# Kernel optimization log

Measured on AMD Instinct MI355X. Metric: run time of the kernel, lower is better.

The kernel has to match this reference:

```python
import jax, jax.numpy as jnp
import numpy as np

P = 8.0  # Lp norm order for NormDist layers (finite-p distance conv)
CHUNK = 8  # output-channel chunk for memory-bounded distance computation
EPS = 8.0 / 255.0


def lp_norm(d, p=P):
    # stable Lp norm over last axis: m * (sum((d/m)^p))^(1/p)
    m = jnp.max(d, axis=-1)
    ms = jnp.where(m > 0, m, 1.0)
    s = jnp.sum((d / ms[..., None]) ** p, axis=-1)
    ss = jnp.where(m > 0, s, 1.0)
    return m * ss ** (1.0 / p)


def extract_patches(t, k, s, pad):
    # [B,C,H,W] -> [B, L, C*k*k] (torch-unfold channel-major ordering), L=Ho*Wo
    pt = jax.lax.conv_general_dilated_patches(t, (k, k), (s, s), [(pad, pad), (pad, pad)])
    B, F, Ho, Wo = pt.shape
    return pt.reshape(B, F, Ho * Wo).transpose(0, 2, 1), Ho, Wo


def normdist_conv(c, lo, hi, w, k, s, pad):
    # Lp-distance conv with interval bound propagation on (center, lower, upper)
    pc, Ho, Wo = extract_patches(c, k, s, pad)
    pl, _, _ = extract_patches(lo, k, s, pad)
    ph, _, _ = extract_patches(hi, k, s, pad)
    O = w.shape[0]
    wf = w.reshape(O, -1)  # [O, F]

    def per_chunk(wc):  # wc: [CHUNK, F]
        dc = jnp.abs(pc[:, :, None, :] - wc)                     # [B,L,CHUNK,F]
        oc = lp_norm(dc)
        # per-element distance bounds given lo <= x <= hi
        dl = jnp.maximum(jnp.maximum(pl[:, :, None, :] - wc, wc - ph[:, :, None, :]), 0.0)
        ol = lp_norm(dl)
        dh = jnp.maximum(jnp.abs(pl[:, :, None, :] - wc), jnp.abs(ph[:, :, None, :] - wc))
        oh = lp_norm(dh)
        return oc, ol, oh

    oc, ol, oh = jax.lax.map(per_chunk, wf.reshape(O // CHUNK, CHUNK, -1))

    def to_img(t):  # [nch, B, L, CHUNK] -> [B, O, Ho, Wo]
        nch, B, L, ch = t.shape
        return t.transpose(1, 0, 3, 2).reshape(B, nch * ch, Ho, Wo)

    return to_img(oc), to_img(ol), to_img(oh)


def bound_relu(c, lo, hi):
    return jax.nn.relu(c), jax.nn.relu(lo), jax.nn.relu(hi)


def _mp(t):
    return jax.lax.reduce_window(t, -jnp.inf, jax.lax.max, (1, 1, 3, 3), (1, 1, 2, 2), 'VALID')


def bound_maxpool(c, lo, hi):
    return _mp(c), _mp(lo), _mp(hi)


def bound_linear(c, lo, hi, W, b=None):
    oc = c @ W.T
    mid = ((lo + hi) * 0.5) @ W.T
    rad = ((hi - lo) * 0.5) @ jnp.abs(W).T
    if b is not None:
        oc = oc + b
        mid = mid + b
    return oc, mid - rad, mid + rad


def setup_inputs() -> dict:
    key = jax.random.key(0)
    ks = jax.random.split(key, 10)
    x = jax.random.normal(ks[0], (16, 3, 32, 32), jnp.float32)
    lower = x - EPS
    upper = x + EPS
    w1 = jax.random.normal(ks[1], (96, 3, 7, 7), jnp.float32)
    w2 = jax.random.normal(ks[2], (256, 96, 5, 5), jnp.float32)
    w3 = jax.random.normal(ks[3], (384, 256, 3, 3), jnp.float32)
    w4 = jax.random.normal(ks[4], (384, 384, 3, 3), jnp.float32)
    w5 = jax.random.normal(ks[5], (256, 384, 3, 3), jnp.float32)
    fw1 = jax.random.normal(ks[6], (1024, 2304), jnp.float32) * 0.02
    fw2 = jax.random.normal(ks[7], (512, 1024), jnp.float32) * 0.03
    fw3 = jax.random.normal(ks[8], (10, 512), jnp.float32) * 0.04
    fb3 = jax.random.normal(ks[9], (10,), jnp.float32)
    return {"x": x, "lower": lower, "upper": upper, "w1": w1, "w2": w2, "w3": w3,
            "w4": w4, "w5": w5, "fw1": fw1, "fw2": fw2, "fw3": fw3, "fb3": fb3}


def reference(x, lower, upper, w1, w2, w3, w4, w5, fw1, fw2, fw3, fb3):
    c, l, u = normdist_conv(x, lower, upper, w1, 7, 2, 2)   # 32 -> 15
    c, l, u = bound_relu(c, l, u)
    c, l, u = bound_maxpool(c, l, u)                        # 15 -> 7
    c, l, u = normdist_conv(c, l, u, w2, 5, 1, 2)           # 7 -> 7
    c, l, u = bound_relu(c, l, u)
    c, l, u = bound_maxpool(c, l, u)                        # 7 -> 3
    c, l, u = normdist_conv(c, l, u, w3, 3, 1, 1)
    c, l, u = bound_relu(c, l, u)
    c, l, u = normdist_conv(c, l, u, w4, 3, 1, 1)
    c, l, u = bound_relu(c, l, u)
    c, l, u = normdist_conv(c, l, u, w5, 3, 1, 1)
    c, l, u = bound_relu(c, l, u)
    B = c.shape[0]
    c, l, u = c.reshape(B, -1), l.reshape(B, -1), u.reshape(B, -1)
    c, l, u = bound_linear(c, l, u, fw1)
    c, l, u = bound_relu(c, l, u)
    c, l, u = bound_linear(c, l, u, fw2)
    c, l, u = bound_relu(c, l, u)
    c, l, u = bound_linear(c, l, u, fw3, fb3)
    # final negation swaps the roles of lower/upper
    return (-c, -u, -l)
```

## Files before the change

### kernel.cpp

```cpp
#include <hip/hip_runtime.h>
#include <math.h>


__device__ __forceinline__ float rt8(float s) { return sqrtf(sqrtf(sqrtf(s))); }

__device__ __forceinline__ void tap16(float w, float pc, float pl, float pu,
                                      float& aC, float& aL, float& aH)
{
    float a = pc - w; float a2 = a * a, a4 = a2 * a2; aC = fmaf(a4, a4, aC);
    float x = pl - w, y = pu - w;
    float dl = fmaxf(fmaxf(x, -y), 0.f);
    float e2 = dl * dl, e4 = e2 * e2; aL = fmaf(e4, e4, aL);
    float h2 = fmaxf(x * x, y * y);
    float h4 = h2 * h2; aH = fmaf(h4, h4, aH);
}

__launch_bounds__(256)
__global__ void wtrans4(const float* __restrict__ W2, const float* __restrict__ W3,
                        const float* __restrict__ W4, const float* __restrict__ W5,
                        float* __restrict__ T2, float* __restrict__ T3,
                        float* __restrict__ T4, float* __restrict__ T5)
{
    constexpr int nt2 = 4 * 38, nt3 = 6 * 36, nt4 = 6 * 54, nt5 = 4 * 54;
    int bid = blockIdx.x;
    const float* W; float* T; int O, CK, t;
    if (bid < nt2)                   { W = W2; T = T2; O = 256; CK = 2400; t = bid; }
    else if (bid < nt2 + nt3)        { W = W3; T = T3; O = 384; CK = 2304; t = bid - nt2; }
    else if (bid < nt2 + nt3 + nt4)  { W = W4; T = T4; O = 384; CK = 3456; t = bid - nt2 - nt3; }
    else                             { W = W5; T = T5; O = 256; CK = 3456; t = bid - nt2 - nt3 - nt4; }
    int tilesC = (CK + 63) / 64;
    int to = t / tilesC, tc = t - to * tilesC;
    int o0 = to * 64, c0 = tc * 64;
    __shared__ float tile[64][65];
    int lane = threadIdx.x & 63, wv = threadIdx.x >> 6;
    #pragma unroll
    for (int i = 0; i < 16; ++i) {
        int row = wv + i * 4;
        int c = c0 + lane;
        tile[row][lane] = (c < CK) ? W[(size_t)(o0 + row) * CK + c] : 0.f;
    }
    __syncthreads();
    #pragma unroll
    for (int i = 0; i < 16; ++i) {
        int row = wv + i * 4;
        int c = c0 + row;
        if (c < CK) T[(size_t)c * O + o0 + lane] = tile[lane][row];
    }
}

template<int K, int S, int PAD, int CC, int HIN, int WIN, int HO, int WO>
__launch_bounds__(256)
__global__ void conv_a(const float* __restrict__ IC, const float* __restrict__ IL,
                       const float* __restrict__ IU, const float* __restrict__ W,
                       float* __restrict__ OUT, int B, int Cin, int O, int OG)
{
    constexpr int PH = (HO - 1) * S + K;
    constexpr int PW = (WO - 1) * S + K;
    constexpr int PP = PH * PW;
    constexpr int HW = HIN * WIN;
    constexpr int NP = HO * WO;
    constexpr int ROUNDS = (NP + 63) / 64;
    __shared__ float lds[CC * 3 * PP];

    int og = blockIdx.x % OG;
    int b  = (blockIdx.x / OG) % B;
    int tid = threadIdx.x;

    for (int i = tid; i < CC * 3 * PP; i += 256) lds[i] = 0.f;
    __syncthreads();
    for (int tsel = 0; tsel < 3; ++tsel) {
        const float* src = (tsel == 0 ? IC : (tsel == 1 ? IL : IU))
                         + (size_t)b * Cin * HW;
        for (int e = tid; e < CC * HW; e += 256) {
            int c = e / HW, p = e % HW;
            int pr = p / WIN, pw_ = p % WIN;
            lds[c * 3 * PP + tsel * PP + (pr + PAD) * PW + (pw_ + PAD)] = src[e];
        }
    }
    __syncthreads();

    int wave = tid >> 6, lane = tid & 63;
    int o = __builtin_amdgcn_readfirstlane(og * 4 + wave);
    const float* wp = W + (size_t)o * Cin * (K * K);

    for (int r = 0; r < ROUNDS; ++r) {
        int pos = r * 64 + lane;
        bool act = pos < NP;
        int pp = act ? pos : 0;
        int oh = pp / WO, ow = pp % WO;
        const float* sl = lds + (oh * S) * PW + ow * S;
        const float* wc = wp;
        float aC = 0.f, aL = 0.f, aH = 0.f;
        for (int c = 0; c < CC; ++c) {
            #pragma unroll
            for (int kh = 0; kh < K; ++kh)
                #pragma unroll
                for (int kw = 0; kw < K; ++kw) {
                    float w = wc[kh * K + kw];
                    tap16(w, sl[kh * PW + kw], sl[PP + kh * PW + kw],
                          sl[2 * PP + kh * PW + kw], aC, aL, aH);
                }
            sl += 3 * PP; wc += K * K;
        }
        if (act) {
            size_t N = (size_t)B * O * NP;
            size_t oidx = ((size_t)b * O + o) * NP + pos;
            OUT[oidx] = aC; OUT[N + oidx] = aL; OUT[2 * N + oidx] = aH;
        }
    }
}

__global__ void pool_rt8(const float* __restrict__ in, float* __restrict__ out,
                         int BC, int Hin, int Win, int Ho, int Wo,
                         int n_in, int n_out)
{
    int idx = blockIdx.x * blockDim.x + threadIdx.x;
    int per = BC * Ho * Wo;
    if (idx >= 3 * per) return;
    int tsel = idx / per; int r = idx - tsel * per;
    int ow = r % Wo; int t2 = r / Wo;
    int oh = t2 % Ho; int bc = t2 / Ho;
    const float* ip = in + (size_t)tsel * n_in + (size_t)bc * Hin * Win;
    int ih0 = oh * 2, iw0 = ow * 2;
    float m = -INFINITY;
    #pragma unroll
    for (int i = 0; i < 3; ++i)
        #pragma unroll
        for (int j = 0; j < 3; ++j)
            m = fmaxf(m, ip[(ih0 + i) * Win + (iw0 + j)]);
    out[(size_t)tsel * n_out + r] = rt8(m);
}

template<int CC>
__launch_bounds__(256)
__global__ void conv2_kernel(const float* __restrict__ IN, const float* __restrict__ WT,
                             float* __restrict__ P, int nin)
{
    constexpr int B = 16, Cin = 96, O = 256;
    constexpr size_t N = (size_t)B * O * 49;
    __shared__ __align__(16) float slab[CC * 180];
    int x = blockIdx.x;
    int oh   = x % 7;
    int b    = (x / 7) % B;
    int chunk = x / (7 * B);
    int c0 = chunk * CC;
    int tid = threadIdx.x;

    for (int i = tid; i < CC * 180; i += 256) {
        int c = i / 180; int rem = i - c * 180;
        int tsel = rem / 60; int rr = rem - tsel * 60;
        int r = rr / 12, col = rr - r * 12;
        int ih = oh + r - 2, iw = col - 2;
        float v = 0.f;
        if (col < 11 && (unsigned)ih < 7u && (unsigned)iw < 7u)
            v = IN[(size_t)tsel * nin + ((size_t)b * Cin + c0 + c) * 49 + ih * 7 + iw];
        slab[i] = v;
    }
    __syncthreads();

    int o = tid;
    float aC[7], aL[7], aH[7];
    #pragma unroll
    for (int u = 0; u < 7; ++u) { aC[u] = 0.f; aL[u] = 0.f; aH[u] = 0.f; }

    for (int c = 0; c < CC; ++c) {
        const float* wp = WT + (size_t)((c0 + c) * 25) * O + o;
        float w[25];
        #pragma unroll
        for (int t = 0; t < 25; ++t) w[t] = wp[(size_t)t * O];
        const float* sb = slab + c * 180;
        #pragma unroll
        for (int r = 0; r < 5; ++r) {
            float X[12], L[12], U[12];
            const float4* px = (const float4*)(sb + r * 12);
            const float4* pl = (const float4*)(sb + 60 + r * 12);
            const float4* pu = (const float4*)(sb + 120 + r * 12);
            ((float4*)X)[0] = px[0]; ((float4*)X)[1] = px[1]; ((float4*)X)[2] = px[2];
            ((float4*)L)[0] = pl[0]; ((float4*)L)[1] = pl[1]; ((float4*)L)[2] = pl[2];
            ((float4*)U)[0] = pu[0]; ((float4*)U)[1] = pu[1]; ((float4*)U)[2] = pu[2];
            #pragma unroll
            for (int ow = 0; ow < 7; ++ow)
                #pragma unroll
                for (int kw = 0; kw < 5; ++kw)
                    tap16(w[r * 5 + kw], X[ow + kw], L[ow + kw], U[ow + kw],
                          aC[ow], aL[ow], aH[ow]);
        }
    }

    float* Pc = P + (size_t)chunk * 3 * N;
    size_t rowbase = ((size_t)(b * 7 + oh) * 7) * O + o;
    #pragma unroll
    for (int u = 0; u < 7; ++u) {
        Pc[rowbase + (size_t)u * O]         = aC[u];
        Pc[N + rowbase + (size_t)u * O]     = aL[u];
        Pc[2 * N + rowbase + (size_t)u * O] = aH[u];
    }
}

__global__ void comb2_pool2(const float* __restrict__ P, float* __restrict__ D)
{
    constexpr int B = 16, O = 256, NCH = 16;
    constexpr size_t N = (size_t)B * O * 49;
    int idx = blockIdx.x * blockDim.x + threadIdx.x;
    if (idx >= 3 * B * 9 * O) return;
    int o = idx & 255; int t = idx >> 8;
    int pos = t % 9; t /= 9;
    int b = t % B; int tsel = t / B;
    int ph = pos / 3, pw = pos % 3;
    float m = 0.f;
    #pragma unroll
    for (int i = 0; i < 3; ++i)
        #pragma unroll
        for (int j = 0; j < 3; ++j) {
            int sp = (ph * 2 + i) * 7 + (pw * 2 + j);
            size_t base = (size_t)tsel * N + ((size_t)b * 49 + sp) * O + o;
            float s = 0.f;
            #pragma unroll
            for (int ch = 0; ch < NCH; ++ch) s += P[(size_t)ch * 3 * N + base];
            m = fmaxf(m, s);
        }
    D[idx] = rt8(m);
}

template<int CC>
__launch_bounds__(384)
__global__ void conv3x3_kernel(const float* __restrict__ IN, const float* __restrict__ WT,
                               float* __restrict__ P, int B, int Cin, int O)
{
    __shared__ float slab[CC * 75];
    int x = blockIdx.x;
    int b = x % B;
    int chunk = x / B;
    int c0 = chunk * CC;
    int tid = threadIdx.x;

    for (int i = tid; i < CC * 75; i += blockDim.x) {
        int c = i / 75; int rem = i - c * 75;
        int tsel = rem / 25; int rr = rem - tsel * 25;
        int iy = rr / 5, ix = rr - iy * 5;
        int ih = iy - 1, iw = ix - 1;
        float v = 0.f;
        if ((unsigned)ih < 3u && (unsigned)iw < 3u)
            v = IN[(((size_t)tsel * B + b) * 9 + (ih * 3 + iw)) * Cin + (c0 + c)];
        slab[i] = v;
    }
    __syncthreads();

    int o = tid;
    float aC[9], aL[9], aH[9];
    #pragma unroll
    for (int u = 0; u < 9; ++u) { aC[u] = 0.f; aL[u] = 0.f; aH[u] = 0.f; }

    for (int c = 0; c < CC; ++c) {
        const float* wp = WT + (size_t)((c0 + c) * 9) * O + o;
        float w[9];
        #pragma unroll
        for (int t = 0; t < 9; ++t) w[t] = wp[(size_t)t * O];
        const float* sb = slab + c * 75;
        #pragma unroll
        for (int py = 0; py < 3; ++py)
            #pragma unroll
            for (int px = 0; px < 3; ++px)
                #pragma unroll
                for (int ky = 0; ky < 3; ++ky)
                    #pragma unroll
                    for (int kx = 0; kx < 3; ++kx) {
                        int iy = py + ky, ix = px + kx;
                        tap16(w[ky * 3 + kx], sb[iy * 5 + ix], sb[25 + iy * 5 + ix],
                              sb[50 + iy * 5 + ix],
                              aC[py * 3 + px], aL[py * 3 + px], aH[py * 3 + px]);
                    }
    }

    size_t N = (size_t)B * O * 9;
    float* Pc = P + (size_t)chunk * 3 * N;
    size_t base = ((size_t)b * 9) * O + o;
    #pragma unroll
    for (int u = 0; u < 9; ++u) {
        Pc[base + (size_t)u * O]         = aC[u];
        Pc[N + base + (size_t)u * O]     = aL[u];
        Pc[2 * N + base + (size_t)u * O] = aH[u];
    }
}

__global__ void conv_comb_flat(const float* __restrict__ P, float* __restrict__ OUT,
                               size_t N3, int NCH)
{
    size_t idx = (size_t)blockIdx.x * blockDim.x + threadIdx.x;
    if (idx >= N3) return;
    float s = 0.f;
    for (int ch = 0; ch < NCH; ++ch) s += P[(size_t)ch * N3 + idx];
    OUT[idx] = rt8(s);
}

__global__ void comb5_std(const float* __restrict__ P, float* __restrict__ G, int NCH)
{
    constexpr int B = 16, O = 256;
    constexpr size_t N = (size_t)B * O * 9;
    size_t idx = (size_t)blockIdx.x * blockDim.x + threadIdx.x;
    if (idx >= 3 * N) return;
    float s = 0.f;
    for (int ch = 0; ch < NCH; ++ch) s += P[(size_t)ch * 3 * N + idx];
    int o = (int)(idx % O); size_t t = idx / O;
    int pos = (int)(t % 9); t /= 9;
    int b = (int)(t % B); int tsel = (int)(t / B);
    G[(size_t)tsel * N + ((size_t)b * O + o) * 9 + pos] = rt8(s);
}

__launch_bounds__(256)
__global__ void fc_gemv(const float* __restrict__ IC, const float* __restrict__ IL,
                        const float* __restrict__ IU, const float* __restrict__ W,
                        float* __restrict__ OUT, int B, int In, int Out)
{
    int gw = (int)((blockIdx.x * blockDim.x + threadIdx.x) >> 6);
    int lane = threadIdx.x & 63;
    if (gw >= B * Out) return;
    int o = gw % Out, b = gw / Out;
    const float4* wr = (const float4*)(W  + (size_t)o * In);
    const float4* cr = (const float4*)(IC + (size_t)b * In);
    const float4* lr = (const float4*)(IL + (size_t)b * In);
    const float4* ur = (const float4*)(IU + (size_t)b * In);
    int In4 = In >> 2;
    float sc = 0.f, sm = 0.f, sr = 0.f;
    for (int i = lane; i < In4; i += 64) {
        float4 w4 = wr[i], c4 = cr[i], l4 = lr[i], u4 = ur[i];
        sc = fmaf(c4.x, w4.x, sc); sc = fmaf(c4.y, w4.y, sc);
        sc = fmaf(c4.z, w4.z, sc); sc = fmaf(c4.w, w4.w, sc);
        sm = fmaf((l4.x + u4.x) * 0.5f, w4.x, sm);
        sm = fmaf((l4.y + u4.y) * 0.5f, w4.y, sm);
        sm = fmaf((l4.z + u4.z) * 0.5f, w4.z, sm);
        sm = fmaf((l4.w + u4.w) * 0.5f, w4.w, sm);
        sr = fmaf((u4.x - l4.x) * 0.5f, fabsf(w4.x), sr);
        sr = fmaf((u4.y - l4.y) * 0.5f, fabsf(w4.y), sr);
        sr = fmaf((u4.z - l4.z) * 0.5f, fabsf(w4.z), sr);
        sr = fmaf((u4.w - l4.w) * 0.5f, fabsf(w4.w), sr);
    }
    #pragma unroll
    for (int off = 32; off; off >>= 1) {
        sc += __shfl_xor(sc, off);
        sm += __shfl_xor(sm, off);
        sr += __shfl_xor(sr, off);
    }
    if (lane == 0) {
        size_t N = (size_t)B * Out;
        size_t idx = (size_t)b * Out + o;
        OUT[idx]         = fmaxf(sc, 0.f);
        OUT[N + idx]     = fmaxf(sm - sr, 0.f);
        OUT[2 * N + idx] = fmaxf(sm + sr, 0.f);
    }
}

__global__ void bound_linear_kernel(
    const float* __restrict__ IC, const float* __restrict__ IL, const float* __restrict__ IU,
    const float* __restrict__ W, const float* __restrict__ bias,
    float* __restrict__ OC, float* __restrict__ OL, float* __restrict__ OU,
    int B, int In, int Out)
{
    int idx = blockIdx.x * blockDim.x + threadIdx.x;
    if (idx >= B * Out) return;
    int o = idx % Out, b = idx / Out;
    const float* wr = W  + (size_t)o * In;
    const float* cr = IC + (size_t)b * In;
    const float* lr = IL + (size_t)b * In;
    const float* ur = IU + (size_t)b * In;
    float sc = 0.f, sm = 0.f, sr = 0.f;
    for (int i = 0; i < In; ++i) {
        float w = wr[i];
        sc = fmaf(cr[i], w, sc);
        sm = fmaf((lr[i] + ur[i]) * 0.5f, w, sm);
        sr = fmaf((ur[i] - lr[i]) * 0.5f, fabsf(w), sr);
    }
    float bb = bias[o]; sc += bb; sm += bb;
    OC[idx] = -sc; OL[idx] = -(sm - sr); OU[idx] = -(sm + sr);
}

extern "C" void kernel_launch(void* const* d_in, const int* in_sizes, int n_in,
                              void* d_out, int out_size, void* d_ws, size_t ws_size,
                              hipStream_t stream)
{
    const float* x   = (const float*)d_in[0];
    const float* lo  = (const float*)d_in[1];
    const float* hi  = (const float*)d_in[2];
    const float* w1  = (const float*)d_in[3];
    const float* w2  = (const float*)d_in[4];
    const float* w3  = (const float*)d_in[5];
    const float* w4  = (const float*)d_in[6];
    const float* w5  = (const float*)d_in[7];
    const float* fw1 = (const float*)d_in[8];
    const float* fw2 = (const float*)d_in[9];
    const float* fw3 = (const float*)d_in[10];
    const float* fb3 = (const float*)d_in[11];
    float* out = (float*)d_out;
    float* ws  = (float*)d_ws;

    const size_t n_c1 = 16u * 96 * 15 * 15;
    const size_t n_p1 = 16u * 96 * 7 * 7;
    const size_t n_d  = 16u * 256 * 9;
    const size_t n_c3 = 16u * 384 * 9;
    const size_t n_c5 = 16u * 256 * 9;
    const size_t n_f1 = 16u * 1024;
    const size_t n_f2 = 16u * 512;

    float* A   = ws;
    float* Bp  = A  + 3 * n_c1;
    float* D   = Bp + 3 * n_p1;
    float* E   = D  + 3 * n_d;
    float* F   = E  + 3 * n_c3;
    float* G   = F  + 3 * n_c3;
    float* H   = G  + 3 * n_c5;
    float* I   = H  + 3 * n_f1;
    float* WT2 = I  + 3 * n_f2;
    float* WT3 = WT2 + 614400;
    float* WT4 = WT3 + 884736;
    float* WT5 = WT4 + 1327104;
    float* SP  = WT5 + 884736;

    const int BS = 256;
    auto grid = [](size_t tot) { return dim3((unsigned)((tot + 255) / 256)); };

    wtrans4<<<4 * 38 + 6 * 36 + 6 * 54 + 4 * 54, BS, 0, stream>>>(
        w2, w3, w4, w5, WT2, WT3, WT4, WT5);

    conv_a<7, 2, 2, 3, 32, 32, 15, 15><<<384, BS, 0, stream>>>(
        x, lo, hi, w1, A, 16, 3, 96, 24);
    pool_rt8<<<grid(3 * n_p1), BS, 0, stream>>>(
        A, Bp, 16 * 96, 15, 15, 7, 7, (int)n_c1, (int)n_p1);
    conv2_kernel<6><<<16 * 16 * 7, 256, 0, stream>>>(Bp, WT2, SP, (int)n_p1);
    comb2_pool2<<<grid(3 * n_d), BS, 0, stream>>>(SP, D);
    conv3x3_kernel<8><<<32 * 16, 384, 0, stream>>>(D, WT3, SP, 16, 256, 384);
    conv_comb_flat<<<grid(3 * n_c3), BS, 0, stream>>>(SP, E, 3 * n_c3, 32);
    conv3x3_kernel<8><<<48 * 16, 384, 0, stream>>>(E, WT4, SP, 16, 384, 384);
    conv_comb_flat<<<grid(3 * n_c3), BS, 0, stream>>>(SP, F, 3 * n_c3, 48);
    conv3x3_kernel<8><<<48 * 16, 256, 0, stream>>>(F, WT5, SP, 16, 384, 256);
    comb5_std<<<grid(3 * n_c5), BS, 0, stream>>>(SP, G, 48);
    fc_gemv<<<grid(16384u * 64), BS, 0, stream>>>(
        G, G + n_c5, G + 2 * n_c5, fw1, H, 16, 2304, 1024);
    fc_gemv<<<grid(8192u * 64), BS, 0, stream>>>(
        H, H + n_f1, H + 2 * n_f1, fw2, I, 16, 1024, 512);
    bound_linear_kernel<<<grid(160), BS, 0, stream>>>(
        I, I + n_f2, I + 2 * n_f2, fw3, fb3,
        out, out + 320, out + 160, 16, 512, 10);
}
```

Baseline: 655.0 us.

## Pack channel pairs into float2 lanes to use packed FP32 math in conv kernels

Weights are transposed into a channel-pair interleaved layout and the input slabs are stored with adjacent channels interleaved. The conv2 and 3x3 kernels then process two input channels per iteration with 2-wide vector types, which lets the compiler emit packed FP32 instructions (v_pk_fma/v_pk_mul). The two lanes are summed at the end. This relies on CC being even and changes the weight layout, and it raises register use for the vector accumulators.

```diff
diff --git a/kernel.cpp b/kernel.cpp
--- a/kernel.cpp
+++ b/kernel.cpp
@@ -1,6 +1,8 @@
 #include <hip/hip_runtime.h>
 #include <math.h>
 
+
+typedef float vf2 __attribute__((ext_vector_type(2)));
 
 __device__ __forceinline__ float rt8(float s) { return sqrtf(sqrtf(sqrtf(s))); }
 
@@ -15,6 +17,21 @@
     float h4 = h2 * h2; aH = fmaf(h4, h4, aH);
 }
 
+__device__ __forceinline__ void tap16v2(vf2 w, vf2 pc, vf2 pl, vf2 pu,
+                                        vf2& aC, vf2& aL, vf2& aH)
+{
+    vf2 a = pc - w; vf2 a2 = a * a, a4 = a2 * a2;
+    aC = __builtin_elementwise_fma(a4, a4, aC);
+    vf2 x = pl - w, y = pu - w;
+    vf2 zero = {0.f, 0.f};
+    vf2 dl = __builtin_elementwise_max(__builtin_elementwise_max(x, -y), zero);
+    vf2 e2 = dl * dl, e4 = e2 * e2;
+    aL = __builtin_elementwise_fma(e4, e4, aL);
+    vf2 h2 = __builtin_elementwise_max(x * x, y * y);
+    vf2 h4 = h2 * h2;
+    aH = __builtin_elementwise_fma(h4, h4, aH);
+}
+
 __launch_bounds__(256)
 __global__ void wtrans4(const float* __restrict__ W2, const float* __restrict__ W3,
                         const float* __restrict__ W4, const float* __restrict__ W5,
@@ -23,11 +40,11 @@
 {
     constexpr int nt2 = 4 * 38, nt3 = 6 * 36, nt4 = 6 * 54, nt5 = 4 * 54;
     int bid = blockIdx.x;
-    const float* W; float* T; int O, CK, t;
-    if (bid < nt2)                   { W = W2; T = T2; O = 256; CK = 2400; t = bid; }
-    else if (bid < nt2 + nt3)        { W = W3; T = T3; O = 384; CK = 2304; t = bid - nt2; }
-    else if (bid < nt2 + nt3 + nt4)  { W = W4; T = T4; O = 384; CK = 3456; t = bid - nt2 - nt3; }
-    else                             { W = W5; T = T5; O = 256; CK = 3456; t = bid - nt2 - nt3 - nt4; }
+    const float* W; float* T; int O, CK, KK, t;
+    if (bid < nt2)                   { W = W2; T = T2; O = 256; CK = 2400; KK = 25; t = bid; }
+    else if (bid < nt2 + nt3)        { W = W3; T = T3; O = 384; CK = 2304; KK = 9; t = bid - nt2; }
+    else if (bid < nt2 + nt3 + nt4)  { W = W4; T = T4; O = 384; CK = 3456; KK = 9; t = bid - nt2 - nt3; }
+    else                             { W = W5; T = T5; O = 256; CK = 3456; KK = 9; t = bid - nt2 - nt3 - nt4; }
     int tilesC = (CK + 63) / 64;
     int to = t / tilesC, tc = t - to * tilesC;
     int o0 = to * 64, c0 = tc * 64;
@@ -43,8 +60,12 @@
     #pragma unroll
     for (int i = 0; i < 16; ++i) {
         int row = wv + i * 4;
-        int c = c0 + row;
-        if (c < CK) T[(size_t)c * O + o0 + lane] = tile[lane][row];
+        int ck = c0 + row;
+        if (ck < CK) {
+            int c = ck / KK, tt = ck - c * KK;
+            T[(size_t)((c >> 1) * KK + tt) * (2 * O) + (size_t)(o0 + lane) * 2 + (c & 1)]
+                = tile[lane][row];
+        }
     }
 }
 
@@ -137,8 +158,9 @@
                              float* __restrict__ P, int nin)
 {
     constexpr int B = 16, Cin = 96, O = 256;
+    constexpr int CP = CC / 2;
     constexpr size_t N = (size_t)B * O * 49;
-    __shared__ __align__(16) float slab[CC * 180];
+    __shared__ __align__(16) float slab[CP * 360];
     int x = blockIdx.x;
     int oh   = x % 7;
     int b    = (x / 7) % B;
@@ -146,44 +168,48 @@
     int c0 = chunk * CC;
     int tid = threadIdx.x;
 
-    for (int i = tid; i < CC * 180; i += 256) {
-        int c = i / 180; int rem = i - c * 180;
-        int tsel = rem / 60; int rr = rem - tsel * 60;
-        int r = rr / 12, col = rr - r * 12;
+    for (int i = tid; i < CP * 360; i += 256) {
+        int cp = i / 360; int rem = i - cp * 360;
+        int tsel = rem / 120; int rr = rem - tsel * 120;
+        int r = rr / 24; int cpar = rr - r * 24;
+        int col = cpar >> 1, par = cpar & 1;
+        int c = c0 + cp * 2 + par;
         int ih = oh + r - 2, iw = col - 2;
         float v = 0.f;
         if (col < 11 && (unsigned)ih < 7u && (unsigned)iw < 7u)
-            v = IN[(size_t)tsel * nin + ((size_t)b * Cin + c0 + c) * 49 + ih * 7 + iw];
+            v = IN[(size_t)tsel * nin + ((size_t)b * Cin + c) * 49 + ih * 7 + iw];
         slab[i] = v;
     }
     __syncthreads();
 
     int o = tid;
-    float aC[7], aL[7], aH[7];
-    #pragma unroll
-    for (int u = 0; u < 7; ++u) { aC[u] = 0.f; aL[u] = 0.f; aH[u] = 0.f; }
-
-    for (int c = 0; c < CC; ++c) {
-        const float* wp = WT + (size_t)((c0 + c) * 25) * O + o;
-        float w[25];
-        #pragma unroll
-        for (int t = 0; t < 25; ++t) w[t] = wp[(size_t)t * O];
-        const float* sb = slab + c * 180;
+    vf2 aC2[7], aL2[7], aH2[7];
+    vf2 zero = {0.f, 0.f};
+    #pragma unroll
+    for (int u = 0; u < 7; ++u) { aC2[u] = zero; aL2[u] = zero; aH2[u] = zero; }
+
+    for (int cp = 0; cp < CP; ++cp) {
+        const float* wp = WT + (size_t)((c0 / 2 + cp) * 25) * (2 * O) + 2 * o;
+        const float* sb = slab + cp * 360;
         #pragma unroll
         for (int r = 0; r < 5; ++r) {
-            float X[12], L[12], U[12];
-            const float4* px = (const float4*)(sb + r * 12);
-            const float4* pl = (const float4*)(sb + 60 + r * 12);
-            const float4* pu = (const float4*)(sb + 120 + r * 12);
-            ((float4*)X)[0] = px[0]; ((float4*)X)[1] = px[1]; ((float4*)X)[2] = px[2];
-            ((float4*)L)[0] = pl[0]; ((float4*)L)[1] = pl[1]; ((float4*)L)[2] = pl[2];
-            ((float4*)U)[0] = pu[0]; ((float4*)U)[1] = pu[1]; ((float4*)U)[2] = pu[2];
+            vf2 wr[5];
+            #pragma unroll
+            for (int kw = 0; kw < 5; ++kw)
+                wr[kw] = *(const vf2*)(wp + (size_t)(r * 5 + kw) * (2 * O));
+            vf2 X[12], L[12], U[12];
+            #pragma unroll
+            for (int i2 = 0; i2 < 12; ++i2) {
+                X[i2] = *(const vf2*)(sb + r * 24 + i2 * 2);
+                L[i2] = *(const vf2*)(sb + 120 + r * 24 + i2 * 2);
+                U[i2] = *(const vf2*)(sb + 240 + r * 24 + i2 * 2);
+            }
             #pragma unroll
             for (int ow = 0; ow < 7; ++ow)
                 #pragma unroll
                 for (int kw = 0; kw < 5; ++kw)
-                    tap16(w[r * 5 + kw], X[ow + kw], L[ow + kw], U[ow + kw],
-                          aC[ow], aL[ow], aH[ow]);
+                    tap16v2(wr[kw], X[ow + kw], L[ow + kw], U[ow + kw],
+                            aC2[ow], aL2[ow], aH2[ow]);
         }
     }
 
@@ -191,9 +217,9 @@
     size_t rowbase = ((size_t)(b * 7 + oh) * 7) * O + o;
     #pragma unroll
     for (int u = 0; u < 7; ++u) {
-        Pc[rowbase + (size_t)u * O]         = aC[u];
-        Pc[N + rowbase + (size_t)u * O]     = aL[u];
-        Pc[2 * N + rowbase + (size_t)u * O] = aH[u];
+        Pc[rowbase + (size_t)u * O]         = aC2[u].x + aC2[u].y;
+        Pc[N + rowbase + (size_t)u * O]     = aL2[u].x + aL2[u].y;
+        Pc[2 * N + rowbase + (size_t)u * O] = aH2[u].x + aH2[u].y;
     }
 }
 
@@ -227,36 +253,40 @@
 __global__ void conv3x3_kernel(const float* __restrict__ IN, const float* __restrict__ WT,
                                float* __restrict__ P, int B, int Cin, int O)
 {
-    __shared__ float slab[CC * 75];
+    constexpr int CP = CC / 2;
+    __shared__ __align__(8) float slab[CP * 150];
     int x = blockIdx.x;
     int b = x % B;
     int chunk = x / B;
     int c0 = chunk * CC;
     int tid = threadIdx.x;
 
-    for (int i = tid; i < CC * 75; i += blockDim.x) {
-        int c = i / 75; int rem = i - c * 75;
-        int tsel = rem / 25; int rr = rem - tsel * 25;
-        int iy = rr / 5, ix = rr - iy * 5;
+    for (int i = tid; i < CP * 150; i += blockDim.x) {
+        int cp = i / 150; int rem = i - cp * 150;
+        int tsel = rem / 50; int rr = rem - tsel * 50;
+        int p = rr >> 1, par = rr & 1;
+        int iy = p / 5, ix = p - iy * 5;
         int ih = iy - 1, iw = ix - 1;
+        int c = c0 + cp * 2 + par;
         float v = 0.f;
         if ((unsigned)ih < 3u && (unsigned)iw < 3u)
-            v = IN[(((size_t)tsel * B + b) * 9 + (ih * 3 + iw)) * Cin + (c0 + c)];
+            v = IN[(((size_t)tsel * B + b) * 9 + (ih * 3 + iw)) * Cin + c];
         slab[i] = v;
     }
     __syncthreads();
 
     int o = tid;
-    float aC[9], aL[9], aH[9];
-    #pragma unroll
-    for (int u = 0; u < 9; ++u) { aC[u] = 0.f; aL[u] = 0.f; aH[u] = 0.f; }
-
-    for (int c = 0; c < CC; ++c) {
-        const float* wp = WT + (size_t)((c0 + c) * 9) * O + o;
-        float w[9];
+    vf2 aC2[9], aL2[9], aH2[9];
+    vf2 zero = {0.f, 0.f};
+    #pragma unroll
+    for (int u = 0; u < 9; ++u) { aC2[u] = zero; aL2[u] = zero; aH2[u] = zero; }
+
+    for (int cp = 0; cp < CP; ++cp) {
+        const float* wp = WT + (size_t)((c0 / 2 + cp) * 9) * (2 * O) + 2 * o;
+        vf2 w2[9];
         #pragma unroll
-        for (int t = 0; t < 9; ++t) w[t] = wp[(size_t)t * O];
-        const float* sb = slab + c * 75;
+        for (int t = 0; t < 9; ++t) w2[t] = *(const vf2*)(wp + (size_t)t * (2 * O));
+        const float* sb = slab + cp * 150;
         #pragma unroll
         for (int py = 0; py < 3; ++py)
             #pragma unroll
@@ -265,10 +295,12 @@
                 for (int ky = 0; ky < 3; ++ky)
                     #pragma unroll
                     for (int kx = 0; kx < 3; ++kx) {
-                        int iy = py + ky, ix = px + kx;
-                        tap16(w[ky * 3 + kx], sb[iy * 5 + ix], sb[25 + iy * 5 + ix],
-                              sb[50 + iy * 5 + ix],
-                              aC[py * 3 + px], aL[py * 3 + px], aH[py * 3 + px]);
+                        int p = (py + ky) * 5 + (px + kx);
+                        tap16v2(w2[ky * 3 + kx],
+                                *(const vf2*)(sb + p * 2),
+                                *(const vf2*)(sb + 50 + p * 2),
+                                *(const vf2*)(sb + 100 + p * 2),
+                                aC2[py * 3 + px], aL2[py * 3 + px], aH2[py * 3 + px]);
                     }
     }
 
@@ -277,9 +309,9 @@
     size_t base = ((size_t)b * 9) * O + o;
     #pragma unroll
     for (int u = 0; u < 9; ++u) {
-        Pc[base + (size_t)u * O]         = aC[u];
-        Pc[N + base + (size_t)u * O]     = aL[u];
-        Pc[2 * N + base + (size_t)u * O] = aH[u];
+        Pc[base + (size_t)u * O]         = aC2[u].x + aC2[u].y;
+        Pc[N + base + (size_t)u * O]     = aL2[u].x + aL2[u].y;
+        Pc[2 * N + base + (size_t)u * O] = aH2[u].x + aH2[u].y;
     }
 }
 
```

Result: faster. 593.6 us (-9.4%).
